# Kernel optimization log

Hardware: AMD Instinct MI355X
Metric: run time of the kernel (lower is better)

The kernel has to match this reference:

```python
import jax, jax.numpy as jnp
import numpy as np

N_NODES = 100000
N_EDGES = 1_600_000
D = 32


def setup_inputs() -> dict:
    key = jax.random.key(0)
    k1, k2, k3, k4, k5 = jax.random.split(key, 5)
    x = jax.random.normal(k1, (N_NODES, D), dtype=jnp.float32)
    W1 = jax.random.normal(k2, (D, D), dtype=jnp.float32) * (1.0 / np.sqrt(D))
    W2 = jax.random.normal(k3, (D, D), dtype=jnp.float32) * (1.0 / np.sqrt(D))
    b2 = jax.random.normal(k4, (D,), dtype=jnp.float32) * 0.01
    edge_index = jax.random.randint(k5, (2, N_EDGES), 0, N_NODES, dtype=jnp.int64)
    return {"x": x, "W1": W1, "W2": W2, "b2": b2, "edge_index": edge_index}


def reference(x, W1, W2, b2, edge_index):
    # ptensors0.transfer0 over the graph: F1[i] = sum_{(j->i) in E} x[j]
    src = edge_index[0]
    dst = edge_index[1]
    F1 = jax.ops.segment_sum(x[src], dst, num_segments=x.shape[0])  # [N, D]
    # out = lin2(x) + lin1(F1)  (lin2 has bias, lin1 does not; torch Linear: y = x @ W.T + b)
    return x @ W2.T + b2 + F1 @ W1.T
```

## Files before the change

### kernel.cpp

```cpp
#include <hip/hip_runtime.h>
#include <hip/hip_bf16.h>

#define DIM 32
#define LOG_NPB 7
#define NPB 128
#define CAP 4096
#define NBINS 800
#define EPB 16384
#define EPT 16

__global__ __launch_bounds__(256) void fused_lin_kernel(
    const float* __restrict__ x,
    const float* __restrict__ W1,
    const float* __restrict__ W2,
    const float* __restrict__ b2,
    float* __restrict__ out,
    unsigned* __restrict__ y32,
    int* __restrict__ cursor, int nb,
    int n_nodes)
{
    __shared__ float W1s[DIM][DIM];
    __shared__ float W2s[DIM][DIM];
    __shared__ float b2s[DIM];
    __shared__ float xs[8][DIM];

    const int t = threadIdx.x;

    if (blockIdx.x == 0) {
        for (int i = t; i < nb; i += 256) cursor[i] = i * CAP;
    }

    for (int i = t; i < DIM * DIM; i += 256) {
        int c = i >> 5, k = i & 31;
        W1s[k][c] = W1[i];
        W2s[k][c] = W2[i];
    }
    if (t < DIM) b2s[t] = b2[t];

    const int r = t >> 5;
    const int c = t & 31;
    const int ntiles = (n_nodes + 7) >> 3;

    for (int tile = blockIdx.x; tile < ntiles; tile += gridDim.x) {
        const int row = tile * 8 + r;
        __syncthreads();
        if (row < n_nodes) xs[r][c] = x[(long)row * DIM + c];
        __syncthreads();
        if (row < n_nodes) {
            float a2 = b2s[c];
            float a1 = 0.0f;
            #pragma unroll
            for (int k = 0; k < DIM; ++k) {
                float xv = xs[r][k];
                a2 += xv * W2s[k][c];
                a1 += xv * W1s[k][c];
            }
            out[(long)row * DIM + c] = a2;
            float hi = __shfl_down(a1, 1);
            if ((c & 1) == 0) {
                __hip_bfloat16 blo = __float2bfloat16(a1);
                __hip_bfloat16 bhi = __float2bfloat16(hi);
                unsigned pack = ((unsigned)(*(unsigned short*)&bhi) << 16)
                              | (unsigned)(*(unsigned short*)&blo);
                y32[(size_t)row * 16 + (c >> 1)] = pack;
            }
        }
    }
}

__global__ __launch_bounds__(1024) void bucket_scatter_kernel(
    const int* __restrict__ src, const int* __restrict__ dst,
    int* __restrict__ cursor, unsigned* __restrict__ bedges, int nE)
{
    __shared__ int cnt[NBINS];
    __shared__ int base[NBINS];

    const int t = threadIdx.x;
    const long blockStart = (long)blockIdx.x * EPB;

    for (int i = t; i < NBINS; i += 1024) cnt[i] = 0;
    __syncthreads();

    int es[EPT], ed[EPT], rk[EPT];
    #pragma unroll
    for (int i = 0; i < EPT; ++i) {
        long e = blockStart + i * 1024 + t;
        if (e < nE) { es[i] = src[e]; ed[i] = dst[e]; }
        else        { es[i] = -1;     ed[i] = 0;      }
    }
    #pragma unroll
    for (int i = 0; i < EPT; ++i) {
        if (es[i] >= 0) rk[i] = atomicAdd(&cnt[ed[i] >> LOG_NPB], 1);
    }
    __syncthreads();

    for (int i = t; i < NBINS; i += 1024) {
        int c = cnt[i];
        if (c > 0) base[i] = atomicAdd(&cursor[i], c);
    }
    __syncthreads();

    #pragma unroll
    for (int i = 0; i < EPT; ++i) {
        if (es[i] >= 0) {
            int b = ed[i] >> LOG_NPB;
            int p = base[b] + rk[i];
            if (p < (b + 1) * CAP)
                bedges[p] = ((unsigned)es[i] << LOG_NPB) | (unsigned)(ed[i] & (NPB - 1));
        }
    }
}

__global__ __launch_bounds__(512) void sort_gather_kernel(
    const int* __restrict__ cursor, const unsigned* __restrict__ bedges,
    const unsigned short* __restrict__ yb,
    float* __restrict__ out, int n_nodes)
{
    __shared__ unsigned ent[CAP];
    __shared__ unsigned sorted[CAP];
    __shared__ int cnt[NPB];
    __shared__ int ex[NPB];
    __shared__ int cur[NPB];

    const int b = blockIdx.x;
    const int t = threadIdx.x;
    const int start = b * CAP;
    int n = cursor[b] - start;
    if (n > CAP) n = CAP;
    if (n < 0) n = 0;

    if (t < NPB) { cnt[t] = 0; cur[t] = 0; }
    __syncthreads();

    for (int i = t; i < n; i += 512) {
        unsigned e = bedges[start + i];
        ent[i] = e;
        atomicAdd(&cnt[e & (NPB - 1)], 1);
    }
    __syncthreads();

    if (t < NPB) ex[t] = cnt[t];
    __syncthreads();
    for (int off = 1; off < NPB; off <<= 1) {
        int add = 0;
        if (t < NPB && t >= off) add = ex[t - off];
        __syncthreads();
        if (t < NPB) ex[t] += add;
        __syncthreads();
    }
    if (t < NPB) ex[t] -= cnt[t];
    __syncthreads();

    for (int i = t; i < n; i += 512) {
        unsigned e = ent[i];
        int bin = (int)(e & (NPB - 1));
        int r = atomicAdd(&cur[bin], 1);
        sorted[ex[bin] + r] = e >> LOG_NPB;
    }
    __syncthreads();

    const int wv   = t >> 6;
    const int lane = t & 63;
    const int slot = lane >> 3;
    const int li   = lane & 7;

    int ln   = wv;
    int node = b * NPB + ln;
    if (node >= n_nodes) return;

    int st = ex[ln];
    int d  = cnt[ln];
    int s[4];
    #pragma unroll
    for (int k = 0; k < 4; ++k) {
        int e = slot + 8 * k;
        int idx = (e < d) ? e : (d > 0 ? d - 1 : 0);
        s[k] = (int)sorted[(d > 0 ? st : 0) + idx];
    }
    float4 o = make_float4(0.f, 0.f, 0.f, 0.f);
    if (slot == 0) o = ((const float4*)(out + ((size_t)node << 5)))[li];

    while (true) {
        ushort4 u[4];
        #pragma unroll
        for (int k = 0; k < 4; ++k) {
            if (8 * k < d)
                u[k] = *(const ushort4*)(yb + ((size_t)s[k] << 5) + (li << 2));
        }

        const int ln_n   = ln + 8;
        const int node_n = node + 8;
        const bool have_n = (ln_n < NPB) && (node_n < n_nodes);
        int st_n = 0, d_n = 0;
        int sn[4];
        float4 o_n = make_float4(0.f, 0.f, 0.f, 0.f);
        if (have_n) {
            st_n = ex[ln_n];
            d_n  = cnt[ln_n];
            #pragma unroll
            for (int k = 0; k < 4; ++k) {
                int e = slot + 8 * k;
                int idx = (e < d_n) ? e : (d_n > 0 ? d_n - 1 : 0);
                sn[k] = (int)sorted[(d_n > 0 ? st_n : 0) + idx];
            }
            if (slot == 0) o_n = ((const float4*)(out + ((size_t)node_n << 5)))[li];
        }

        float a0 = 0.f, a1 = 0.f, a2 = 0.f, a3 = 0.f;
        #pragma unroll
        for (int k = 0; k < 4; ++k) {
            if (8 * k < d) {
                const bool v = (slot + 8 * k) < d;
                a0 += v ? __uint_as_float((unsigned)u[k].x << 16) : 0.f;
                a1 += v ? __uint_as_float((unsigned)u[k].y << 16) : 0.f;
                a2 += v ? __uint_as_float((unsigned)u[k].z << 16) : 0.f;
                a3 += v ? __uint_as_float((unsigned)u[k].w << 16) : 0.f;
            }
        }
        for (int e0 = 32 + slot; e0 < d; e0 += 8) {
            int ss = (int)sorted[st + e0];
            ushort4 uu = *(const ushort4*)(yb + ((size_t)ss << 5) + (li << 2));
            a0 += __uint_as_float((unsigned)uu.x << 16);
            a1 += __uint_as_float((unsigned)uu.y << 16);
            a2 += __uint_as_float((unsigned)uu.z << 16);
            a3 += __uint_as_float((unsigned)uu.w << 16);
        }

        #pragma unroll
        for (int m = 8; m < 64; m <<= 1) {
            a0 += __shfl_xor(a0, m);
            a1 += __shfl_xor(a1, m);
            a2 += __shfl_xor(a2, m);
            a3 += __shfl_xor(a3, m);
        }

        if (slot == 0 && d > 0) {
            float4 w;
            w.x = o.x + a0; w.y = o.y + a1; w.z = o.z + a2; w.w = o.w + a3;
            ((float4*)(out + ((size_t)node << 5)))[li] = w;
        }

        if (!have_n) break;
        ln = ln_n; node = node_n; st = st_n; d = d_n;
        s[0] = sn[0]; s[1] = sn[1]; s[2] = sn[2]; s[3] = sn[3];
        o = o_n;
    }
}

extern "C" void kernel_launch(void* const* d_in, const int* in_sizes, int n_in,
                              void* d_out, int out_size, void* d_ws, size_t ws_size,
                              hipStream_t stream) {
    const float* x  = (const float*)d_in[0];
    const float* W1 = (const float*)d_in[1];
    const float* W2 = (const float*)d_in[2];
    const float* b2 = (const float*)d_in[3];
    const int*   ei = (const int*)d_in[4];

    const int n_nodes = in_sizes[0] / DIM;
    const int n_edges = in_sizes[4] / 2;
    const int* src = ei;
    const int* dst = ei + n_edges;
    float* out = (float*)d_out;

    const int nb = (n_nodes + NPB - 1) / NPB;

    char* basep = (char*)d_ws;
    size_t off = 0;
    auto alloc = [&](size_t bytes) {
        char* p = basep + off;
        off = (off + bytes + 255) & ~(size_t)255;
        return p;
    };
    unsigned* y32    = (unsigned*)alloc((size_t)n_nodes * DIM * sizeof(unsigned short));
    int*      cursor = (int*)     alloc((size_t)nb * sizeof(int));
    unsigned* bedges = (unsigned*)alloc((size_t)nb * CAP * sizeof(unsigned));
    (void)ws_size;

    fused_lin_kernel<<<1024, 256, 0, stream>>>(x, W1, W2, b2, out, y32, cursor, nb, n_nodes);
    bucket_scatter_kernel<<<(n_edges + EPB - 1) / EPB, 1024, 0, stream>>>(src, dst, cursor, bedges, n_edges);
    sort_gather_kernel<<<nb, 512, 0, stream>>>(cursor, bedges, (const unsigned short*)y32, out, n_nodes);
}
```

Before: 81.63 us.

## Stage bucketed edges in shared memory for coalesced global writes

The edge bucketing kernel now counts bins in a first pass, then builds an exclusive scan and places each packed edge into a shared-memory staging buffer grouped by bin. Each wavefront then copies whole bin segments contiguously to global memory, replacing the scattered per-edge global writes with coalesced runs. The block is shrunk to 12K edges so the stage fits in LDS. In exchange, src/dst are read from global twice, the kernel adds several barriers and a 1024-wide scan, and the larger LDS footprint may reduce occupancy.

```diff
diff --git a/kernel.cpp b/kernel.cpp
--- a/kernel.cpp
+++ b/kernel.cpp
@@ -6,8 +6,8 @@
 #define NPB 128
 #define CAP 4096
 #define NBINS 800
-#define EPB 16384
-#define EPT 16
+#define EPB 12288
+#define EPT 12
 
 __global__ __launch_bounds__(256) void fused_lin_kernel(
     const float* __restrict__ x,
@@ -72,8 +72,11 @@
     const int* __restrict__ src, const int* __restrict__ dst,
     int* __restrict__ cursor, unsigned* __restrict__ bedges, int nE)
 {
+    __shared__ unsigned stage[EPB];
     __shared__ int cnt[NBINS];
-    __shared__ int base[NBINS];
+    __shared__ int ex[NBINS];
+    __shared__ int gbase[NBINS];
+    __shared__ int scanbuf[1024];
 
     const int t = threadIdx.x;
     const long blockStart = (long)blockIdx.x * EPB;
@@ -81,33 +84,57 @@
     for (int i = t; i < NBINS; i += 1024) cnt[i] = 0;
     __syncthreads();
 
-    int es[EPT], ed[EPT], rk[EPT];
     #pragma unroll
     for (int i = 0; i < EPT; ++i) {
-        long e = blockStart + i * 1024 + t;
-        if (e < nE) { es[i] = src[e]; ed[i] = dst[e]; }
-        else        { es[i] = -1;     ed[i] = 0;      }
-    }
+        long e = blockStart + (long)i * 1024 + t;
+        if (e < nE) atomicAdd(&cnt[dst[e] >> LOG_NPB], 1);
+    }
+    __syncthreads();
+
+    int v = (t < NBINS) ? cnt[t] : 0;
+    scanbuf[t] = v;
+    __syncthreads();
+    for (int off = 1; off < 1024; off <<= 1) {
+        int add = (t >= off) ? scanbuf[t - off] : 0;
+        __syncthreads();
+        scanbuf[t] += add;
+        __syncthreads();
+    }
+    if (t < NBINS) ex[t] = scanbuf[t] - v;
+    __syncthreads();
+
+    for (int b = t; b < NBINS; b += 1024) {
+        int c = cnt[b];
+        if (c > 0) gbase[b] = atomicAdd(&cursor[b], c);
+    }
+    scanbuf[t] = 0;
+    __syncthreads();
+
     #pragma unroll
     for (int i = 0; i < EPT; ++i) {
-        if (es[i] >= 0) rk[i] = atomicAdd(&cnt[ed[i] >> LOG_NPB], 1);
-    }
-    __syncthreads();
-
-    for (int i = t; i < NBINS; i += 1024) {
-        int c = cnt[i];
-        if (c > 0) base[i] = atomicAdd(&cursor[i], c);
-    }
-    __syncthreads();
-
-    #pragma unroll
-    for (int i = 0; i < EPT; ++i) {
-        if (es[i] >= 0) {
-            int b = ed[i] >> LOG_NPB;
-            int p = base[b] + rk[i];
-            if (p < (b + 1) * CAP)
-                bedges[p] = ((unsigned)es[i] << LOG_NPB) | (unsigned)(ed[i] & (NPB - 1));
-        }
+        long e = blockStart + (long)i * 1024 + t;
+        if (e < nE) {
+            int es = src[e];
+            int ed = dst[e];
+            int b  = ed >> LOG_NPB;
+            int r  = atomicAdd(&scanbuf[b], 1);
+            stage[ex[b] + r] = ((unsigned)es << LOG_NPB) | (unsigned)(ed & (NPB - 1));
+        }
+    }
+    __syncthreads();
+
+    const int wv   = t >> 6;
+    const int lane = t & 63;
+    for (int b = wv; b < NBINS; b += 16) {
+        int c = cnt[b];
+        if (c == 0) continue;
+        int lbase = ex[b];
+        int gb    = gbase[b];
+        int cmax  = (b + 1) * CAP - gb;
+        if (cmax < 0) cmax = 0;
+        if (c > cmax) c = cmax;
+        for (int j = lane; j < c; j += 64)
+            bedges[gb + j] = stage[lbase + j];
     }
 }
 
```

Result: slower. 89.12 us (+9.2%).
